# Kernel tuning notes

Hardware: AMD Instinct MI355X
Metric: run time of the kernel (lower is better)

## Reference

```python
import jax, jax.numpy as jnp
import numpy as np
from jax import lax

DIM = 4096
N_HEADS = 32
N_KV_HEADS = 8
HEAD_DIM = DIM // N_HEADS  # 128
N_REP = N_HEADS // N_KV_HEADS  # 4
B, S = 1, 2048
ROPE_THETA = 10000.0
NEG_INF = -1e9


def setup_inputs() -> dict:
    key = jax.random.key(0)
    ks = jax.random.split(key, 6)
    scale = 1.0 / np.sqrt(DIM)
    x = jax.random.normal(ks[0], (B, S, DIM), dtype=jnp.float32)
    wq = jax.random.normal(ks[1], (DIM, DIM), dtype=jnp.float32) * scale
    wk = jax.random.normal(ks[2], (N_KV_HEADS * HEAD_DIM, DIM), dtype=jnp.float32) * scale
    wv = jax.random.normal(ks[3], (N_KV_HEADS * HEAD_DIM, DIM), dtype=jnp.float32) * scale
    wo = jax.random.normal(ks[4], (DIM, DIM), dtype=jnp.float32) * scale
    # Llama rotary frequencies: freqs_cis[t, i] = exp(i * t * theta^(-2i/d))
    inv_freq = 1.0 / (ROPE_THETA ** (np.arange(0, HEAD_DIM, 2, dtype=np.float32) / HEAD_DIM))
    angles = np.outer(np.arange(S, dtype=np.float32), inv_freq)  # [S, HEAD_DIM//2]
    freqs_cos = jnp.asarray(np.cos(angles), dtype=jnp.float32)
    freqs_sin = jnp.asarray(np.sin(angles), dtype=jnp.float32)
    cache_k = jnp.zeros((B, S, N_KV_HEADS, HEAD_DIM), dtype=jnp.float32)
    cache_v = jnp.zeros((B, S, N_KV_HEADS, HEAD_DIM), dtype=jnp.float32)
    # causal mask added to scores (broadcasts over [B, H, S, S])
    mask = jnp.where(np.triu(np.ones((S, S), dtype=bool), k=1), NEG_INF, 0.0).astype(jnp.float32)
    return {"x": x, "wq": wq, "wk": wk, "wv": wv, "wo": wo,
            "freqs_cos": freqs_cos, "freqs_sin": freqs_sin,
            "cache_k": cache_k, "cache_v": cache_v, "mask": mask,
            "start_pos": 0}


def _apply_rotary(t, cos, sin):
    # t: [B, S, H, HEAD_DIM]; cos/sin: [S, HEAD_DIM//2]
    b, s, h, d = t.shape
    tr = t.reshape(b, s, h, d // 2, 2)
    a, bb = tr[..., 0], tr[..., 1]  # real / imag of consecutive pairs
    c = cos[None, :, None, :]
    sn = sin[None, :, None, :]
    out_r = a * c - bb * sn
    out_i = a * sn + bb * c
    return jnp.stack([out_r, out_i], axis=-1).reshape(b, s, h, d)


def reference(x, wq, wk, wv, wo, freqs_cos, freqs_sin, cache_k, cache_v, mask, start_pos):
    bsz, seqlen, _ = x.shape
    xq = jnp.einsum('bsd,od->bso', x, wq).reshape(bsz, seqlen, N_HEADS, HEAD_DIM)
    xk = jnp.einsum('bsd,od->bso', x, wk).reshape(bsz, seqlen, N_KV_HEADS, HEAD_DIM)
    xv = jnp.einsum('bsd,od->bso', x, wv).reshape(bsz, seqlen, N_KV_HEADS, HEAD_DIM)
    xq = _apply_rotary(xq, freqs_cos, freqs_sin)
    xk = _apply_rotary(xk, freqs_cos, freqs_sin)
    # KV-cache append
    cache_k = lax.dynamic_update_slice(cache_k, xk, (0, start_pos, 0, 0))
    cache_v = lax.dynamic_update_slice(cache_v, xv, (0, start_pos, 0, 0))
    kv_len = start_pos + seqlen
    keys = cache_k[:, :kv_len]    # [B, KVLEN, KV, HD]
    values = cache_v[:, :kv_len]
    # GQA: repeat_interleave over kv heads
    keys = jnp.repeat(keys, N_REP, axis=2)      # [B, KVLEN, H, HD]
    values = jnp.repeat(values, N_REP, axis=2)
    q = xq.transpose(0, 2, 1, 3)       # [B, H, S, HD]
    k = keys.transpose(0, 2, 1, 3)     # [B, H, KVLEN, HD]
    v = values.transpose(0, 2, 1, 3)
    scores = jnp.einsum('bhqd,bhkd->bhqk', q, k) / np.sqrt(HEAD_DIM)
    scores = scores + mask[None, None, :, :]
    probs = jax.nn.softmax(scores.astype(jnp.float32), axis=-1).astype(q.dtype)
    out = jnp.einsum('bhqk,bhkd->bhqd', probs, v)
    out = out.transpose(0, 2, 1, 3).reshape(bsz, seqlen, -1)
    return jnp.einsum('bso,do->bsd', out, wo)
```

## Files before the change

kernel.cpp:

```cpp
#include <hip/hip_runtime.h>
#include <hip/hip_bf16.h>

typedef unsigned short u16;
typedef unsigned int u32;
typedef __bf16 bf16x8 __attribute__((ext_vector_type(8)));
typedef float f32x4 __attribute__((ext_vector_type(4)));
typedef u32 u32x4 __attribute__((ext_vector_type(4)));

#define QKV_LD 6144
#define KOFF 4096
#define VOFF 5120
#define HD 128
#define DIM 4096

__device__ __forceinline__ u16 f2bf(float f) {
  union { __hip_bfloat16 h; u16 u; } c;
  c.h = __float2bfloat16(f);
  return c.u;
}
__device__ __forceinline__ float bf2f(u16 u) {
  union { u16 u; __hip_bfloat16 h; } c;
  c.u = u;
  return __bfloat162float(c.h);
}

typedef __attribute__((address_space(1))) const u32 gas_u32;
typedef __attribute__((address_space(3))) u32 las_u32;
__device__ __forceinline__ void async16(const u16* g, u16* l) {
  __builtin_amdgcn_global_load_lds((gas_u32*)g, (las_u32*)l, 16, 0, 0);
}

__device__ __forceinline__ void store_out(u16* p, float v) { *p = f2bf(v); }
__device__ __forceinline__ void store_out(float* p, float v) { *p = v; }

__global__ __launch_bounds__(256) void cvt_kernel(const float* __restrict__ src,
                                                  u16* __restrict__ dst, int n8) {
  int i = blockIdx.x * 256 + threadIdx.x;
  if (i >= n8) return;
  const f32x4* s4 = (const f32x4*)src;
  f32x4 a = s4[2 * i], b = s4[2 * i + 1];
  u32x4 o;
  o[0] = (u32)f2bf(a[0]) | ((u32)f2bf(a[1]) << 16);
  o[1] = (u32)f2bf(a[2]) | ((u32)f2bf(a[3]) << 16);
  o[2] = (u32)f2bf(b[0]) | ((u32)f2bf(b[1]) << 16);
  o[3] = (u32)f2bf(b[2]) | ((u32)f2bf(b[3]) << 16);
  ((u32x4*)dst)[i] = o;
}

template <typename OutT>
__global__ __launch_bounds__(256, 2) void gemm_nt(const u16* __restrict__ A,
                                                  const u16* __restrict__ B,
                                                  OutT* __restrict__ C, int N, int K) {
  __shared__ u16 As[128 * 32];
  __shared__ u16 Bs[128 * 32];
  const int tid = threadIdx.x;
  const int wave = tid >> 6;
  const int lane = tid & 63;
  const int quad = lane >> 4;
  const int l16 = lane & 15;
  const int bm = blockIdx.y;
  const int bn = blockIdx.x;
  const int wm = (wave >> 1) * 64;
  const int wn = (wave & 1) * 64;

  f32x4 acc[4][4];
#pragma unroll
  for (int i = 0; i < 4; ++i)
#pragma unroll
    for (int j = 0; j < 4; ++j) {
      f32x4 z = {0.f, 0.f, 0.f, 0.f};
      acc[i][j] = z;
    }

  const int srow0 = wave * 32 + (lane >> 2);
  const int scol = (((lane & 3) ^ ((lane >> 2) & 3)) * 8);
  u16* ldsA0 = &As[(wave * 2 + 0) * 512];
  u16* ldsA1 = &As[(wave * 2 + 1) * 512];
  u16* ldsB0 = &Bs[(wave * 2 + 0) * 512];
  u16* ldsB1 = &Bs[(wave * 2 + 1) * 512];
  const u16* Ag0 = A + (size_t)(bm * 128 + srow0) * K + scol;
  const u16* Ag1 = A + (size_t)(bm * 128 + srow0 + 16) * K + scol;
  const u16* Bg0 = B + (size_t)(bn * 128 + srow0) * K + scol;
  const u16* Bg1 = B + (size_t)(bn * 128 + srow0 + 16) * K + scol;

  int aoff[4], boff[4];
#pragma unroll
  for (int mi = 0; mi < 4; ++mi)
    aoff[mi] = (wm + mi * 16 + l16) * 32 + ((quad ^ (l16 & 3)) * 8);
#pragma unroll
  for (int ni = 0; ni < 4; ++ni)
    boff[ni] = (wn + ni * 16 + l16) * 32 + ((quad ^ (l16 & 3)) * 8);

  for (int k0 = 0; k0 < K; k0 += 32) {
    __syncthreads();
    async16(Ag0 + k0, ldsA0);
    async16(Ag1 + k0, ldsA1);
    async16(Bg0 + k0, ldsB0);
    async16(Bg1 + k0, ldsB1);
    __syncthreads();
    bf16x8 af[4], bb[4];
#pragma unroll
    for (int mi = 0; mi < 4; ++mi) af[mi] = *(const bf16x8*)&As[aoff[mi]];
#pragma unroll
    for (int ni = 0; ni < 4; ++ni) bb[ni] = *(const bf16x8*)&Bs[boff[ni]];
#pragma unroll
    for (int mi = 0; mi < 4; ++mi)
#pragma unroll
      for (int ni = 0; ni < 4; ++ni)
        acc[mi][ni] = __builtin_amdgcn_mfma_f32_16x16x32_bf16(af[mi], bb[ni], acc[mi][ni], 0, 0, 0);
  }

#pragma unroll
  for (int mi = 0; mi < 4; ++mi) {
    int row = bm * 128 + wm + mi * 16 + quad * 4;
#pragma unroll
    for (int ni = 0; ni < 4; ++ni) {
      int col = bn * 128 + wn + ni * 16 + l16;
#pragma unroll
      for (int r = 0; r < 4; ++r)
        store_out(&C[(size_t)(row + r) * N + col], acc[mi][ni][r]);
    }
  }
}

__global__ __launch_bounds__(256) void rope_kernel(u16* qkv, const float* __restrict__ fcos,
                                                   const float* __restrict__ fsin) {
  int idx = blockIdx.x * 256 + threadIdx.x;
  int row, colbase, fi;
  if (idx < 2048 * 2048) {
    row = idx >> 11;
    int pi = idx & 2047;
    fi = pi & 63;
    colbase = (pi >> 6) * 128 + fi * 2;
  } else {
    int j = idx - 2048 * 2048;
    row = j >> 9;
    int pj = j & 511;
    fi = pj & 63;
    colbase = KOFF + (pj >> 6) * 128 + fi * 2;
  }
  float c = fcos[row * 64 + fi], s = fsin[row * 64 + fi];
  u32* p = (u32*)(qkv + (size_t)row * QKV_LD + colbase);
  u32 v = *p;
  float a = bf2f((u16)(v & 0xffffu));
  float b = bf2f((u16)(v >> 16));
  float xr = a * c - b * s;
  float xi = a * s + b * c;
  *p = (u32)f2bf(xr) | ((u32)f2bf(xi) << 16);
}

__global__ __launch_bounds__(256) void vtrans_kernel(const u16* __restrict__ qkv,
                                                     u16* __restrict__ vt) {
  __shared__ u16 Ls[64 * 72];
  const int tid = threadIdx.x;
  const int st = blockIdx.x, dt = blockIdx.y, kvh = blockIdx.z;
#pragma unroll
  for (int t = 0; t < 2; ++t) {
    int g = t * 256 + tid;
    int s = g >> 3, c = g & 7;
    u32x4 v = *(const u32x4*)(qkv + (size_t)(st * 64 + s) * QKV_LD + VOFF + kvh * HD + dt * 64 + c * 8);
    *(u32x4*)&Ls[s * 72 + c * 8] = v;
  }
  __syncthreads();
#pragma unroll
  for (int t = 0; t < 2; ++t) {
    int g = t * 256 + tid;
    int d = g >> 3, c2 = g & 7;
    u32x4 o;
#pragma unroll
    for (int j = 0; j < 4; ++j) {
      u16 lo = Ls[(c2 * 8 + 2 * j) * 72 + d];
      u16 hi = Ls[(c2 * 8 + 2 * j + 1) * 72 + d];
      o[j] = (u32)lo | ((u32)hi << 16);
    }
    *(u32x4*)(vt + (size_t)(kvh * HD + dt * 64 + d) * 2048 + st * 64 + c2 * 8) = o;
  }
}

__global__ __launch_bounds__(256, 2) void flash_kernel(const u16* __restrict__ qkv,
                                                       const u16* __restrict__ vt,
                                                       u16* __restrict__ attnb) {
  __shared__ u16 Kl[2][64 * 128];
  __shared__ u16 VtL[2][128 * 64];
  __shared__ u16 Pl[4][16 * 72];
  const int tid = threadIdx.x;
  const int wave = tid >> 6;
  const int lane = tid & 63;
  const int quad = lane >> 4;
  const int l16 = lane & 15;
  const int lid = blockIdx.x;
  const int h = lid & 31;
  const int z = lid >> 5;
  const int qt = (z < 8) ? z : 23 - z;
  const int kvh = h >> 2;
  const float scale = 0.08838834764831845f;
  const int nkt = 2 * qt + 2;

  const int krow_l = (lane >> 4);
  const int kcol_l = (lane & 15);
  const int vd_l = (lane >> 3);
  const int vc = (lane & 7) ^ ((lane >> 3) & 7);

  const u16* kbase = qkv + (size_t)KOFF + kvh * HD;
  const u16* vbase = vt + (size_t)kvh * HD * 2048;

  bf16x8 qf[2][4];
#pragma unroll
  for (int mi = 0; mi < 2; ++mi) {
    const u16* qp = qkv + (size_t)(qt * 128 + wave * 32 + mi * 16 + l16) * QKV_LD + h * HD + quad * 8;
#pragma unroll
    for (int ks = 0; ks < 4; ++ks) qf[mi][ks] = *(const bf16x8*)(qp + ks * 32);
  }

  f32x4 o[2][8];
#pragma unroll
  for (int mi = 0; mi < 2; ++mi)
#pragma unroll
    for (int i = 0; i < 8; ++i) { f32x4 zz = {0.f, 0.f, 0.f, 0.f}; o[mi][i] = zz; }
  float lacc[2] = {0.f, 0.f};

#pragma unroll
  for (int t = 0; t < 4; ++t) {
    int i = wave * 4 + t;
    int row = i * 4 + krow_l;
    int c = kcol_l ^ (row & 15);
    async16(kbase + (size_t)row * QKV_LD + c * 8, &Kl[0][i * 512]);
  }
#pragma unroll
  for (int t = 0; t < 4; ++t) {
    int i = wave * 4 + t;
    int d = i * 8 + vd_l;
    async16(vbase + (size_t)d * 2048 + vc * 8, &VtL[0][i * 512]);
  }

  for (int kt = 0; kt < nkt; ++kt) {
    const int cur = kt & 1;
    __syncthreads();

    f32x4 s4[2][4];
#pragma unroll
    for (int mi = 0; mi < 2; ++mi)
#pragma unroll
      for (int nb = 0; nb < 4; ++nb) { f32x4 zz = {0.f, 0.f, 0.f, 0.f}; s4[mi][nb] = zz; }
#pragma unroll
    for (int nb = 0; nb < 4; ++nb) {
#pragma unroll
      for (int ks = 0; ks < 4; ++ks) {
        int rr = nb * 16 + l16;
        int cc = ((ks * 4 + quad) ^ l16) * 8;
        bf16x8 kf = *(const bf16x8*)&Kl[cur][rr * 128 + cc];
        s4[0][nb] = __builtin_amdgcn_mfma_f32_16x16x32_bf16(qf[0][ks], kf, s4[0][nb], 0, 0, 0);
        s4[1][nb] = __builtin_amdgcn_mfma_f32_16x16x32_bf16(qf[1][ks], kf, s4[1][nb], 0, 0, 0);
      }
    }

    bf16x8 vb[16];
#pragma unroll
    for (int db = 0; db < 8; ++db) {
      int dd = db * 16 + l16;
#pragma unroll
      for (int ks2 = 0; ks2 < 2; ++ks2) {
        int c = (ks2 * 4 + quad) ^ (dd & 7);
        vb[db * 2 + ks2] = *(const bf16x8*)&VtL[cur][dd * 64 + c * 8];
      }
    }

    float p[2][4][4];
    const bool diag = (kt >= 2 * qt);
    if (diag) {
#pragma unroll
      for (int mi = 0; mi < 2; ++mi)
#pragma unroll
        for (int nb = 0; nb < 4; ++nb) {
          int col = kt * 64 + nb * 16 + l16;
#pragma unroll
          for (int r = 0; r < 4; ++r) {
            int row = qt * 128 + wave * 32 + mi * 16 + quad * 4 + r;
            p[mi][nb][r] = (col > row) ? 0.f : __expf(s4[mi][nb][r] * scale);
          }
        }
    } else {
#pragma unroll
      for (int mi = 0; mi < 2; ++mi)
#pragma unroll
        for (int nb = 0; nb < 4; ++nb)
#pragma unroll
          for (int r = 0; r < 4; ++r)
            p[mi][nb][r] = __expf(s4[mi][nb][r] * scale);
    }

    bf16x8 pa[2][2];
#pragma unroll
    for (int mi = 0; mi < 2; ++mi) {
#pragma unroll
      for (int nb = 0; nb < 4; ++nb)
#pragma unroll
        for (int r = 0; r < 4; ++r)
          Pl[wave][(quad * 4 + r) * 72 + nb * 16 + l16] = f2bf(p[mi][nb][r]);
      __asm__ __volatile__("s_waitcnt lgkmcnt(0)" ::: "memory");
#pragma unroll
      for (int ks2 = 0; ks2 < 2; ++ks2)
        pa[mi][ks2] = *(const bf16x8*)&Pl[wave][l16 * 72 + ks2 * 32 + quad * 8];
    }

#pragma unroll
    for (int mi = 0; mi < 2; ++mi) {
      float sm = 0.f;
#pragma unroll
      for (int ks2 = 0; ks2 < 2; ++ks2)
#pragma unroll
        for (int j = 0; j < 8; ++j) sm += (float)pa[mi][ks2][j];
      sm += __shfl_xor(sm, 16);
      sm += __shfl_xor(sm, 32);
      lacc[mi] += sm;
    }

    if (kt + 1 < nkt) {
      const u16* kb = kbase + (size_t)(kt + 1) * 64 * QKV_LD;
      const u16* vb2 = vbase + (kt + 1) * 64;
#pragma unroll
      for (int t = 0; t < 4; ++t) {
        int i = wave * 4 + t;
        int row = i * 4 + krow_l;
        int c = kcol_l ^ (row & 15);
        async16(kb + (size_t)row * QKV_LD + c * 8, &Kl[1 - cur][i * 512]);
      }
#pragma unroll
      for (int t = 0; t < 4; ++t) {
        int i = wave * 4 + t;
        int d = i * 8 + vd_l;
        async16(vb2 + (size_t)d * 2048 + vc * 8, &VtL[1 - cur][i * 512]);
      }
    }

#pragma unroll
    for (int mi = 0; mi < 2; ++mi)
#pragma unroll
      for (int db = 0; db < 8; ++db)
#pragma unroll
        for (int ks2 = 0; ks2 < 2; ++ks2)
          o[mi][db] = __builtin_amdgcn_mfma_f32_16x16x32_bf16(pa[mi][ks2], vb[db * 2 + ks2], o[mi][db], 0, 0, 0);
  }

  float* lsh = (float*)&Pl[wave][0];
  if (quad == 0) {
    lsh[l16] = lacc[0];
    lsh[16 + l16] = lacc[1];
  }
  __asm__ __volatile__("s_waitcnt lgkmcnt(0)" ::: "memory");
  __builtin_amdgcn_wave_barrier();
  f32x4 inv[2];
#pragma unroll
  for (int mi = 0; mi < 2; ++mi) {
    f32x4 lv = *(const f32x4*)&lsh[mi * 16 + quad * 4];
#pragma unroll
    for (int r = 0; r < 4; ++r) inv[mi][r] = 1.f / lv[r];
  }
#pragma unroll
  for (int mi = 0; mi < 2; ++mi)
#pragma unroll
    for (int db = 0; db < 8; ++db)
#pragma unroll
      for (int r = 0; r < 4; ++r) {
        int row = qt * 128 + wave * 32 + mi * 16 + quad * 4 + r;
        int col = h * HD + db * 16 + l16;
        attnb[(size_t)row * DIM + col] = f2bf(o[mi][db][r] * inv[mi][r]);
      }
}

extern "C" void kernel_launch(void* const* d_in, const int* in_sizes, int n_in,
                              void* d_out, int out_size, void* d_ws, size_t ws_size,
                              hipStream_t stream) {
  (void)in_sizes; (void)n_in; (void)out_size; (void)ws_size;
  const float* x    = (const float*)d_in[0];
  const float* wq   = (const float*)d_in[1];
  const float* wk   = (const float*)d_in[2];
  const float* wv   = (const float*)d_in[3];
  const float* wo   = (const float*)d_in[4];
  const float* fcos = (const float*)d_in[5];
  const float* fsin = (const float*)d_in[6];
  float* out = (float*)d_out;

  char* ws = (char*)d_ws;
  u16* xb    = (u16*)(ws);
  u16* wqkvb = (u16*)(ws + (size_t)16777216);
  u16* wob   = (u16*)(ws + (size_t)67108864);
  u16* qkv   = (u16*)(ws + (size_t)100663296);
  u16* attnb = (u16*)(ws + (size_t)125829120);
  u16* vtb   = (u16*)(ws);

  cvt_kernel<<<4096, 256, 0, stream>>>(x, xb, 1048576);
  cvt_kernel<<<8192, 256, 0, stream>>>(wq, wqkvb, 2097152);
  cvt_kernel<<<2048, 256, 0, stream>>>(wk, wqkvb + 16777216, 524288);
  cvt_kernel<<<2048, 256, 0, stream>>>(wv, wqkvb + 20971520, 524288);
  cvt_kernel<<<8192, 256, 0, stream>>>(wo, wob, 2097152);

  gemm_nt<u16><<<dim3(48, 16), 256, 0, stream>>>(xb, wqkvb, qkv, 6144, 4096);
  vtrans_kernel<<<dim3(32, 2, 8), 256, 0, stream>>>(qkv, vtb);
  rope_kernel<<<20480, 256, 0, stream>>>(qkv, fcos, fsin);
  flash_kernel<<<512, 256, 0, stream>>>(qkv, vtb, attnb);
  gemm_nt<float><<<dim3(32, 16), 256, 0, stream>>>(attnb, wob, out, 4096, 4096);
}
```

Baseline: 553.2 us.

## Add 256x256 eight-wave pipelined GEMM with XCD remap for QKV projection

```diff
diff --git a/kernel.cpp b/kernel.cpp
--- a/kernel.cpp
+++ b/kernel.cpp
@@ -121,6 +121,163 @@
         store_out(&C[(size_t)(row + r) * N + col], acc[mi][ni][r]);
     }
   }
+}
+
+#define BAR8 __builtin_amdgcn_s_barrier()
+#define LGKM0                                                     \
+  do {                                                            \
+    asm volatile("s_waitcnt lgkmcnt(0)" ::: "memory");            \
+    __builtin_amdgcn_sched_barrier(0);                            \
+  } while (0)
+#define VMC(n)                                                    \
+  do {                                                            \
+    asm volatile("s_waitcnt vmcnt(" #n ")" ::: "memory");         \
+    __builtin_amdgcn_sched_barrier(0);                            \
+  } while (0)
+
+#define LDA8(buf, half, arr)                                                     \
+  _Pragma("unroll") for (int mi = 0; mi < 4; ++mi) {                             \
+    const int r_ = wm * 64 + mi * 16 + l16;                                      \
+    const u16* p_ = &lds[buf][half][r_ * 64];                                    \
+    _Pragma("unroll") for (int ks = 0; ks < 2; ++ks)                             \
+      arr[mi][ks] = *(const bf16x8*)(p_ + (((ks * 4 + quad) ^ (r_ & 7)) << 3));  \
+  }
+
+#define LDB8(buf, half, arr)                                                     \
+  _Pragma("unroll") for (int ni = 0; ni < 2; ++ni) {                             \
+    const int r_ = wn * 32 + ni * 16 + l16;                                      \
+    const u16* p_ = &lds[buf][2 + (half)][r_ * 64];                              \
+    _Pragma("unroll") for (int ks = 0; ks < 2; ++ks)                             \
+      arr[ni][ks] = *(const bf16x8*)(p_ + (((ks * 4 + quad) ^ (r_ & 7)) << 3));  \
+  }
+
+#define MMA8(qm, qn, af, bf)                                                       \
+  __builtin_amdgcn_s_setprio(1);                                                   \
+  _Pragma("unroll") for (int mi = 0; mi < 4; ++mi)                                 \
+  _Pragma("unroll") for (int ni = 0; ni < 2; ++ni)                                 \
+  _Pragma("unroll") for (int ks = 0; ks < 2; ++ks)                                 \
+    acc[(qm) * 4 + mi][(qn) * 2 + ni] = __builtin_amdgcn_mfma_f32_16x16x32_bf16(   \
+        af[mi][ks], bf[ni][ks], acc[(qm) * 4 + mi][(qn) * 2 + ni], 0, 0, 0);       \
+  __builtin_amdgcn_s_setprio(0);
+
+template <typename OutT>
+__global__ __launch_bounds__(512, 2) void gemm_nt8(const u16* __restrict__ A,
+                                                   const u16* __restrict__ B,
+                                                   OutT* __restrict__ C,
+                                                   int N, int K, int MT) {
+  __shared__ u16 lds[2][4][128 * 64];
+  const int tid = threadIdx.x;
+  const int wave = tid >> 6;
+  const int lane = tid & 63;
+  const int quad = lane >> 4;
+  const int l16 = lane & 15;
+  const int wm = wave >> 2;
+  const int wn = wave & 3;
+
+  const int nwg = gridDim.x;
+  const int bid = blockIdx.x;
+  const int qq = nwg >> 3, rr8 = nwg & 7, xcd = bid & 7, off = bid >> 3;
+  const int wg = (xcd < rr8 ? xcd * (qq + 1) : rr8 * (qq + 1) + (xcd - rr8) * qq) + off;
+  const int bm = wg % MT;
+  const int bn = wg / MT;
+
+  const int NIT = K >> 7;
+
+  const int srow = (wave << 3) + (lane >> 3);
+  const int sgran = (lane & 7) ^ ((lane >> 3) & 7);
+  const u16* Abase = A + (size_t)(bm * 256 + srow) * K + sgran * 8;
+  const u16* Bbase = B + (size_t)(bn * 256 + srow) * K + sgran * 8;
+
+  auto stage = [&](const u16* base, int h, int kt, u16* slot) {
+    const u16* g = base + (size_t)(h * 128) * K + kt * 64;
+    u16* s = slot + wave * (8 * 64);
+    async16(g, s);
+    async16(g + (size_t)64 * K, s + 64 * 64);
+  };
+
+  f32x4 acc[8][4];
+#pragma unroll
+  for (int i = 0; i < 8; ++i)
+#pragma unroll
+    for (int j = 0; j < 4; ++j) {
+      f32x4 z = {0.f, 0.f, 0.f, 0.f};
+      acc[i][j] = z;
+    }
+
+  stage(Abase, 0, 0, &lds[0][0][0]);
+  stage(Bbase, 0, 0, &lds[0][2][0]);
+  stage(Bbase, 1, 0, &lds[0][3][0]);
+  stage(Abase, 1, 0, &lds[0][1][0]);
+  stage(Abase, 0, 1, &lds[1][0][0]);
+  stage(Bbase, 0, 1, &lds[1][2][0]);
+  stage(Bbase, 1, 1, &lds[1][3][0]);
+  VMC(6);
+  BAR8;
+
+  bf16x8 a0[4][2], a1[4][2], b0[2][2], b1[2][2];
+  for (int it = 0; it < NIT; ++it) {
+    const int t2 = 2 * it + 2, t3 = 2 * it + 3;
+    const bool more = (it + 1 < NIT);
+
+    LDA8(0, 0, a0);
+    LDB8(0, 0, b0);
+    stage(Abase, 1, 2 * it + 1, &lds[1][1][0]);
+    BAR8; LGKM0;
+    MMA8(0, 0, a0, b0);
+    BAR8;
+    LDB8(0, 1, b1);
+    if (more) stage(Abase, 0, t2, &lds[0][0][0]);
+    BAR8; LGKM0;
+    MMA8(0, 1, a0, b1);
+    BAR8;
+    LDA8(0, 1, a1);
+    if (more) stage(Bbase, 0, t2, &lds[0][2][0]);
+    BAR8; LGKM0;
+    MMA8(1, 1, a1, b1);
+    BAR8;
+    if (more) stage(Bbase, 1, t2, &lds[0][3][0]);
+    BAR8; LGKM0;
+    MMA8(1, 0, a1, b0);
+    if (more) { VMC(6); } else { VMC(0); }
+    BAR8;
+    LDA8(1, 0, a0);
+    LDB8(1, 0, b0);
+    if (more) stage(Abase, 1, t2, &lds[0][1][0]);
+    BAR8; LGKM0;
+    MMA8(0, 0, a0, b0);
+    BAR8;
+    LDB8(1, 1, b1);
+    if (more) stage(Abase, 0, t3, &lds[1][0][0]);
+    BAR8; LGKM0;
+    MMA8(0, 1, a0, b1);
+    BAR8;
+    LDA8(1, 1, a1);
+    if (more) stage(Bbase, 0, t3, &lds[1][2][0]);
+    BAR8; LGKM0;
+    MMA8(1, 1, a1, b1);
+    BAR8;
+    if (more) stage(Bbase, 1, t3, &lds[1][3][0]);
+    BAR8; LGKM0;
+    MMA8(1, 0, a1, b0);
+    if (more) { VMC(6); } else { VMC(0); }
+    BAR8;
+  }
+
+#pragma unroll
+  for (int qm = 0; qm < 2; ++qm)
+#pragma unroll
+    for (int mi = 0; mi < 4; ++mi) {
+      int row = bm * 256 + qm * 128 + wm * 64 + mi * 16 + quad * 4;
+#pragma unroll
+      for (int qn = 0; qn < 2; ++qn)
+#pragma unroll
+        for (int ni = 0; ni < 2; ++ni) {
+          int col = bn * 256 + qn * 128 + wn * 32 + ni * 16 + l16;
+#pragma unroll
+          for (int r = 0; r < 4; ++r)
+            store_out(&C[(size_t)(row + r) * N + col], acc[qm * 4 + mi][qn * 2 + ni][r]);
+        }
+    }
 }
 
 __global__ __launch_bounds__(256) void rope_kernel(u16* qkv, const float* __restrict__ fcos,
@@ -395,7 +552,7 @@
   cvt_kernel<<<2048, 256, 0, stream>>>(wv, wqkvb + 20971520, 524288);
   cvt_kernel<<<8192, 256, 0, stream>>>(wo, wob, 2097152);
 
-  gemm_nt<u16><<<dim3(48, 16), 256, 0, stream>>>(xb, wqkvb, qkv, 6144, 4096);
+  gemm_nt8<u16><<<dim3(192), 512, 0, stream>>>(xb, wqkvb, qkv, 6144, 4096, 8);
   vtrans_kernel<<<dim3(32, 2, 8), 256, 0, stream>>>(qkv, vtb);
   rope_kernel<<<20480, 256, 0, stream>>>(qkv, fcos, fsin);
   flash_kernel<<<512, 256, 0, stream>>>(qkv, vtb, attnb);
```

Result: no change. 550.5 us (-0.5%).
